# Performance work log

Hardware: AMD Instinct MI355X
Metric: run time of the kernel (lower is better)

## Reference

```python
import jax, jax.numpy as jnp
import numpy as np

CHOOSE_K = 256
NUM_CLASSES = 100
ALPHA = 0.1  # teacher-loss margin (Kaiser et al.)
EPS = 1e-12


def setup_inputs() -> dict:
    key = jax.random.key(0)
    k1, k2, k3, k4 = jax.random.split(key, 4)
    B, D, M, C = 512, 256, 131072, 100
    x = jax.random.normal(k1, (B, D), dtype=jnp.float32)
    y = jax.random.randint(k2, (B,), 0, C)
    mem_keys = jax.random.normal(k3, (M, D), dtype=jnp.float32)
    mem_vals = jax.random.randint(k4, (M,), 0, C)
    return {"x": x, "y": y, "mem_keys": mem_keys, "mem_vals": mem_vals}


def reference(x, y, mem_keys, mem_vals):
    # L2-normalize queries and memory keys (cosine similarity memory)
    qn = x / (jnp.linalg.norm(x, axis=-1, keepdims=True) + EPS)          # [B, D]
    kn = mem_keys / (jnp.linalg.norm(mem_keys, axis=-1, keepdims=True) + EPS)  # [M, D]

    sims = jnp.einsum('bd,md->bm', qn, kn)                                # [B, M]
    top_sims, top_idx = jax.lax.top_k(sims, CHOOSE_K)                     # [B, K]
    top_labels = mem_vals[top_idx]                                        # [B, K]

    # nearest-neighbor label
    closest_label = top_labels[:, 0]                                      # [B]

    # softmax over top-k similarities, scattered into class buckets
    w = jax.nn.softmax(top_sims, axis=-1)                                 # [B, K]
    onehot = jax.nn.one_hot(top_labels, NUM_CLASSES, dtype=w.dtype)       # [B, K, C]
    probs = jnp.einsum('bk,bkc->bc', w, onehot)                           # [B, C]

    # teacher loss: margin between nearest negative and nearest positive neighbor
    pos = top_labels == y[:, None]                                        # [B, K]
    sim_pos = jnp.max(jnp.where(pos, top_sims, -2.0), axis=1)             # [B]
    sim_neg = jnp.max(jnp.where(~pos, top_sims, -2.0), axis=1)            # [B]
    teacher_loss = jax.nn.relu(sim_neg - sim_pos + ALPHA)                 # [B]

    return closest_label, probs, teacher_loss
```

## Files before the change

### kernel.cpp

```cpp
#include <hip/hip_runtime.h>
#include <hip/hip_bf16.h>

#define NB 512
#define ND 256
#define NM 131072
#define NC 100
#define KTOP 256
#define ALPHA 0.1f
#define EPSN 1e-12
#define THRESH 0.155f
#define CUTBAND 0.012f
#define LCH 24
#define NCH 128
#define NSLOT (NCH*LCH)
#define IDXMASK 0x1FFFFu

typedef __attribute__((ext_vector_type(8))) short bf16x8;
typedef __attribute__((ext_vector_type(4))) float f32x4;

__global__ void zero_out_kernel(float* __restrict__ out, int n) {
    int t = blockIdx.x * blockDim.x + threadIdx.x;
    if (t < n) out[t] = 0.0f;
}

static __device__ __forceinline__ unsigned pk2(float a, float b) {
    __hip_bfloat16 ha = __float2bfloat16(a);
    __hip_bfloat16 hb = __float2bfloat16(b);
    unsigned short ua = __builtin_bit_cast(unsigned short, ha);
    unsigned short ub = __builtin_bit_cast(unsigned short, hb);
    return (unsigned)ua | ((unsigned)ub << 16);
}

static __device__ __forceinline__ void gload16(const void* g, const void* l) {
    __builtin_amdgcn_global_load_lds(
        (const __attribute__((address_space(1))) unsigned int*)g,
        (__attribute__((address_space(3))) unsigned int*)l, 16, 0, 0);
}

__global__ void norms_kernel(const float* __restrict__ x, const float* __restrict__ keys,
                             float* __restrict__ rnq32, float* __restrict__ rnk32,
                             double* __restrict__ rnq64, double* __restrict__ rnk64,
                             unsigned short* __restrict__ kb16) {
    int wave = (blockIdx.x * blockDim.x + threadIdx.x) >> 6;
    int lane = threadIdx.x & 63;
    if (wave >= NB + NM) return;
    const float* src = (wave < NB) ? (x + (size_t)wave * ND)
                                   : (keys + (size_t)(wave - NB) * ND);
    float4 v = ((const float4*)src)[lane];
    if (kb16 && wave >= NB) {
        size_t r = (size_t)(wave - NB);
        int kb = (lane << 3) ^ (((int)r & 7) << 4);
        *(uint2*)((char*)kb16 + (r << 9) + kb) =
            make_uint2(pk2(v.x, v.y), pk2(v.z, v.w));
    }
    double s = (double)v.x * v.x + (double)v.y * v.y
             + (double)v.z * v.z + (double)v.w * v.w;
    #pragma unroll
    for (int off = 32; off > 0; off >>= 1) s += __shfl_down(s, off);
    if (lane == 0) {
        double r = 1.0 / (sqrt(s) + EPSN);
        if (wave < NB) { rnq32[wave] = (float)r; rnq64[wave] = r; }
        else           { rnk32[wave - NB] = (float)r; rnk64[wave - NB] = r; }
    }
}

__global__ __launch_bounds__(512) void gemm_filter_pipe(
    const float* __restrict__ x, const unsigned short* __restrict__ kb16,
    const float* __restrict__ rnq, const float* __restrict__ rnk,
    float* __restrict__ cval, unsigned* __restrict__ cidx) {
    __shared__ unsigned short ks3[3][32 * 256];
    __shared__ unsigned lcnt[128];

    int tid  = threadIdx.x;
    int lane = tid & 63;
    int wv   = tid >> 6;
    int wr   = wv >> 1;
    int wc   = (wv & 1) * 16;
    int l15  = lane & 15;
    int lhi  = lane >> 4;
    int kxor = (l15 & 7) << 4;
    int chunk = blockIdx.x;
    int m0    = blockIdx.y * 128;

    if (tid < 128) lcnt[tid] = 0;

    bf16x8 af[2][8];
    #pragma unroll
    for (int mi = 0; mi < 2; ++mi) {
        const float* qp = x + (size_t)(m0 + wr * 32 + mi * 16 + l15) * ND;
        #pragma unroll
        for (int k8 = 0; k8 < 8; ++k8) {
            float4 qa = *(const float4*)(qp + k8 * 32 + lhi * 8);
            float4 qb = *(const float4*)(qp + k8 * 32 + lhi * 8 + 4);
            uint4 uu = make_uint4(pk2(qa.x, qa.y), pk2(qa.z, qa.w),
                                  pk2(qb.x, qb.y), pk2(qb.z, qb.w));
            af[mi][k8] = __builtin_bit_cast(bf16x8, uu);
        }
    }
    float rq[2][4];
    #pragma unroll
    for (int mi = 0; mi < 2; ++mi)
        #pragma unroll
        for (int j = 0; j < 4; ++j)
            rq[mi][j] = rnq[m0 + wr * 32 + mi * 16 + lhi * 4 + j];

    const char* kroot = (const char*)kb16 + ((size_t)chunk << 19);
    int sbase = wv << 11;

    #define STAGEP(T, B)                                                        \
    {                                                                           \
        const char* kb_ = kroot + ((size_t)(T) << 14);                          \
        gload16(kb_ + sbase + (lane << 4),        (const char*)&ks3[(B)][0] + sbase);        \
        gload16(kb_ + sbase + 1024 + (lane << 4), (const char*)&ks3[(B)][0] + sbase + 1024); \
    }

    #define COMPUTEP(T, BC)                                                     \
    {                                                                           \
        int n0 = chunk * 1024 + (T) * 32;                                       \
        const char* bb = (const char*)&ks3[(BC)][0];                            \
        f32x4 acc0 = {}, acc1 = {};                                             \
        _Pragma("unroll")                                                       \
        for (int k8 = 0; k8 < 8; ++k8) {                                        \
            int addr = ((wc + l15) << 9) + (((k8 << 6) + (lhi << 4)) ^ kxor);   \
            bf16x8 bg = *(const bf16x8*)(bb + addr);                            \
            acc0 = __builtin_amdgcn_mfma_f32_16x16x32_bf16(af[0][k8], bg, acc0, 0, 0, 0); \
            acc1 = __builtin_amdgcn_mfma_f32_16x16x32_bf16(af[1][k8], bg, acc1, 0, 0, 0); \
        }                                                                       \
        float rk = rnk[n0 + wc + l15];                                          \
        unsigned key = (unsigned)(n0 + wc + l15);                               \
        _Pragma("unroll")                                                       \
        for (int j = 0; j < 4; ++j) {                                           \
            float s0 = acc0[j] * rq[0][j] * rk;                                 \
            float s1 = acc1[j] * rq[1][j] * rk;                                 \
            int rl0 = wr * 32 + lhi * 4 + j;                                    \
            if (s0 > THRESH) {                                                  \
                unsigned p = atomicAdd(&lcnt[rl0], 1u);                         \
                if (p < LCH) {                                                  \
                    size_t slot = (size_t)(m0 + rl0) * NSLOT + (size_t)chunk * LCH + p; \
                    cval[slot] = s0; cidx[slot] = key;                          \
                }                                                               \
            }                                                                   \
            if (s1 > THRESH) {                                                  \
                unsigned p = atomicAdd(&lcnt[rl0 + 16], 1u);                    \
                if (p < LCH) {                                                  \
                    size_t slot = (size_t)(m0 + rl0 + 16) * NSLOT + (size_t)chunk * LCH + p; \
                    cval[slot] = s1; cidx[slot] = key;                          \
                }                                                               \
            }                                                                   \
        }                                                                       \
    }

    STAGEP(0, 0);
    STAGEP(1, 1);

    int bs = 2, bc = 0;
    for (int t = 0; t < 31; ++t) {
        asm volatile("s_waitcnt vmcnt(2)" ::: "memory");
        __builtin_amdgcn_sched_barrier(0);
        asm volatile("s_barrier" ::: "memory");
        __builtin_amdgcn_sched_barrier(0);
        COMPUTEP(t, bc);
        bc = (bc == 2) ? 0 : bc + 1;
        if (t < 30) {
            STAGEP(t + 2, bs);
            bs = (bs == 2) ? 0 : bs + 1;
        }
    }
    asm volatile("s_waitcnt vmcnt(0)" ::: "memory");
    __builtin_amdgcn_sched_barrier(0);
    asm volatile("s_barrier" ::: "memory");
    __builtin_amdgcn_sched_barrier(0);
    COMPUTEP(31, bc);
    __syncthreads();

    #undef STAGEP
    #undef COMPUTEP

    if (tid < 128) {
        unsigned c = lcnt[tid]; if (c > LCH) c = LCH;
        size_t base = (size_t)(m0 + tid) * NSLOT + (size_t)chunk * LCH;
        for (unsigned p = c; p < LCH; ++p) { cval[base + p] = -2.0f; cidx[base + p] = 0u; }
    }
}

#define LDKF 264

__global__ __launch_bounds__(512) void gemm_filter(
    const float* __restrict__ x, const float* __restrict__ keys,
    const float* __restrict__ rnq, const float* __restrict__ rnk,
    float* __restrict__ cval, unsigned* __restrict__ cidx) {
    __shared__ unsigned short ks[128][LDKF];
    __shared__ unsigned lcnt[128];

    int tid  = threadIdx.x;
    int lane = tid & 63;
    int wv   = tid >> 6;
    int wr4  = (wv >> 1) * 32;
    int wc2  = (wv &  1) * 64;
    int l15  = lane & 15;
    int lhi  = lane >> 4;
    int chunk = blockIdx.x;
    int m0    = blockIdx.y * 128;

    if (tid < 128) lcnt[tid] = 0;

    bf16x8 af[2][8];
    #pragma unroll
    for (int mi = 0; mi < 2; ++mi) {
        const float* qp = x + (size_t)(m0 + wr4 + mi * 16 + l15) * ND;
        #pragma unroll
        for (int k8 = 0; k8 < 8; ++k8) {
            float4 qa = *(const float4*)(qp + k8 * 32 + lhi * 8);
            float4 qb = *(const float4*)(qp + k8 * 32 + lhi * 8 + 4);
            uint4 uu = make_uint4(pk2(qa.x, qa.y), pk2(qa.z, qa.w),
                                  pk2(qb.x, qb.y), pk2(qb.z, qb.w));
            af[mi][k8] = __builtin_bit_cast(bf16x8, uu);
        }
    }
    float rq[2][4];
    #pragma unroll
    for (int mi = 0; mi < 2; ++mi)
        #pragma unroll
        for (int j = 0; j < 4; ++j)
            rq[mi][j] = rnq[m0 + wr4 + mi * 16 + lhi * 4 + j];

    for (int sub = 0; sub < 8; ++sub) {
        int n0 = chunk * 1024 + sub * 128;
        #pragma unroll 8
        for (int it = 0; it < 16; ++it) {
            int f = tid + it * 512;
            int r = f >> 6;
            int c4 = (f & 63) << 2;
            float4 kv = *(const float4*)(keys + (size_t)(n0 + r) * ND + c4);
            *(uint2*)&ks[r][c4] = make_uint2(pk2(kv.x, kv.y), pk2(kv.z, kv.w));
        }
        __syncthreads();

        f32x4 acc[2][4] = {};
        #pragma unroll
        for (int k8 = 0; k8 < 8; ++k8) {
            int ko = k8 * 32 + lhi * 8;
            bf16x8 bg[4];
            #pragma unroll
            for (int ni = 0; ni < 4; ++ni)
                bg[ni] = *(const bf16x8*)&ks[wc2 + ni * 16 + l15][ko];
            #pragma unroll
            for (int mi = 0; mi < 2; ++mi)
                #pragma unroll
                for (int ni = 0; ni < 4; ++ni)
                    acc[mi][ni] = __builtin_amdgcn_mfma_f32_16x16x32_bf16(
                        af[mi][k8], bg[ni], acc[mi][ni], 0, 0, 0);
        }

        float rk[4];
        #pragma unroll
        for (int ni = 0; ni < 4; ++ni) rk[ni] = rnk[n0 + wc2 + ni * 16 + l15];

        #pragma unroll
        for (int mi = 0; mi < 2; ++mi) {
            #pragma unroll
            for (int j = 0; j < 4; ++j) {
                int rl = wr4 + mi * 16 + lhi * 4 + j;
                #pragma unroll
                for (int ni = 0; ni < 4; ++ni) {
                    float sim = acc[mi][ni][j] * rq[mi][j] * rk[ni];
                    if (sim > THRESH) {
                        unsigned p = atomicAdd(&lcnt[rl], 1u);
                        if (p < LCH) {
                            size_t slot = (size_t)(m0 + rl) * NSLOT + (size_t)chunk * LCH + p;
                            cval[slot] = sim;
                            cidx[slot] = (unsigned)(n0 + wc2 + ni * 16 + l15);
                        }
                    }
                }
            }
        }
        __syncthreads();
    }

    if (tid < 128) {
        unsigned c = lcnt[tid]; if (c > LCH) c = LCH;
        size_t base = (size_t)(m0 + tid) * NSLOT + (size_t)chunk * LCH;
        for (unsigned p = c; p < LCH; ++p) { cval[base + p] = -2.0f; cidx[base + p] = 0u; }
    }
}

__global__ __launch_bounds__(512) void finalize(
    const float* __restrict__ cval, const unsigned* __restrict__ cidx,
    const float* __restrict__ x, const float* __restrict__ keys,
    const double* __restrict__ rnq64, const double* __restrict__ rnk64,
    const int* __restrict__ mem_vals, const int* __restrict__ yv,
    float* __restrict__ out) {
    int row = blockIdx.x;
    int tid = threadIdx.x;
    int lane = tid & 63;
    int wv8  = tid >> 6;

    __shared__ double xqd[ND];
    __shared__ double dval[NSLOT];
    __shared__ unsigned skid[NSLOT];
    __shared__ unsigned char flag[NSLOT];
    __shared__ unsigned hist[256];
    __shared__ unsigned eqlist[256];
    __shared__ float bins[128];
    __shared__ double wred_v[8];
    __shared__ unsigned wred_i[8];
    __shared__ double wred_se[8], wred_sp[8], wred_sn[8];
    __shared__ unsigned long long sh_prefix;
    __shared__ unsigned sh_k, eqcnt, ncand;
    __shared__ unsigned selA, kA;
    __shared__ float s_cut;
    __shared__ double s_vm;
    __shared__ unsigned s_im;
    __shared__ float s_se;
    __shared__ double s_sp, s_sn;

    if (tid == 0) {
        ncand = 0; eqcnt = 0; sh_k = KTOP; sh_prefix = 0x3F00000000000000ull;
        selA = 0xFFFFFFFFu; s_cut = 0.0f;
    }
    if (tid < 64) {
        float4 q = ((const float4*)(x + (size_t)row * ND))[tid];
        xqd[tid * 4 + 0] = (double)q.x; xqd[tid * 4 + 1] = (double)q.y;
        xqd[tid * 4 + 2] = (double)q.z; xqd[tid * 4 + 3] = (double)q.w;
    }
    __syncthreads();

    double rq = rnq64[row];

    if (tid < 256) hist[tid] = 0;
    __syncthreads();
    for (int i = tid; i < NSLOT; i += 512) {
        float v = cval[(size_t)row * NSLOT + i];
        if (v > 0.0f) atomicAdd(&hist[(__float_as_uint(v) >> 23) & 255u], 1u);
    }
    __syncthreads();
    for (int off = 1; off < 256; off <<= 1) {
        unsigned vv = 0;
        if (tid < 256) vv = hist[tid] + ((tid + off < 256) ? hist[tid + off] : 0u);
        __syncthreads();
        if (tid < 256) hist[tid] = vv;
        __syncthreads();
    }
    if (tid < 256) {
        unsigned rh = hist[tid];
        unsigned rn = (tid < 255) ? hist[tid + 1] : 0u;
        if (rh >= KTOP && rn < KTOP) { selA = (unsigned)tid; kA = KTOP - rn; }
    }
    __syncthreads();
    if (selA != 0xFFFFFFFFu) {
        unsigned sA = selA, kk = kA;
        if (tid < 256) hist[tid] = 0;
        __syncthreads();
        for (int i = tid; i < NSLOT; i += 512) {
            float v = cval[(size_t)row * NSLOT + i];
            if (v > 0.0f) {
                unsigned u = __float_as_uint(v);
                if (((u >> 23) & 255u) == sA) atomicAdd(&hist[(u >> 15) & 255u], 1u);
            }
        }
        __syncthreads();
        for (int off = 1; off < 256; off <<= 1) {
            unsigned vv = 0;
            if (tid < 256) vv = hist[tid] + ((tid + off < 256) ? hist[tid + off] : 0u);
            __syncthreads();
            if (tid < 256) hist[tid] = vv;
            __syncthreads();
        }
        if (tid < 256) {
            unsigned rh = hist[tid];
            unsigned rn = (tid < 255) ? hist[tid + 1] : 0u;
            if (rh >= kk && rn < kk)
                s_cut = __uint_as_float((sA << 23) | ((unsigned)tid << 15));
        }
        __syncthreads();
    }
    float cutf = (selA != 0xFFFFFFFFu) ? (s_cut - CUTBAND) : 0.0f;

    for (int i = tid; i < NSLOT; i += 512) {
        float v = cval[(size_t)row * NSLOT + i];
        if (v > cutf) {
            unsigned p = atomicAdd(&ncand, 1u);
            skid[p] = cidx[(size_t)row * NSLOT + i] & IDXMASK;
        }
    }
    __syncthreads();
    int nc = (int)ncand;

    for (int c0 = tid * 2; c0 < nc; c0 += 1024) {
        int c1 = c0 + 1;
        bool h1 = (c1 < nc);
        unsigned id0 = skid[c0];
        unsigned id1 = h1 ? skid[c1] : id0;
        const float* kp0 = keys + (size_t)id0 * ND;
        const float* kp1 = keys + (size_t)id1 * ND;
        double a0 = 0, a1 = 0, a2 = 0, a3 = 0;
        double b0 = 0, b1 = 0, b2 = 0, b3 = 0;
        #pragma unroll 4
        for (int d = 0; d < ND; d += 4) {
            float4 kv0 = *(const float4*)(kp0 + d);
            float4 kv1 = *(const float4*)(kp1 + d);
            double x0 = xqd[d + 0], x1 = xqd[d + 1], x2 = xqd[d + 2], x3 = xqd[d + 3];
            a0 = fma(x0, (double)kv0.x, a0);
            a1 = fma(x1, (double)kv0.y, a1);
            a2 = fma(x2, (double)kv0.z, a2);
            a3 = fma(x3, (double)kv0.w, a3);
            b0 = fma(x0, (double)kv1.x, b0);
            b1 = fma(x1, (double)kv1.y, b1);
            b2 = fma(x2, (double)kv1.z, b2);
            b3 = fma(x3, (double)kv1.w, b3);
        }
        dval[c0] = ((a0 + a1) + (a2 + a3)) * rq * rnk64[id0];
        if (h1) dval[c1] = ((b0 + b1) + (b2 + b3)) * rq * rnk64[id1];
    }
    __syncthreads();

    for (int pass = 1; pass < 8; ++pass) {
        int shift = 56 - pass * 8;
        unsigned long long mask_hi = ~0ull << (shift + 8);
        unsigned long long pfx = sh_prefix;
        unsigned kcur = sh_k;
        if (tid < 256) hist[tid] = 0;
        __syncthreads();
        for (int c = tid; c < nc; c += 512) {
            unsigned long long u = (unsigned long long)__double_as_longlong(dval[c]);
            if ((u & mask_hi) == pfx)
                atomicAdd(&hist[(unsigned)(u >> shift) & 255u], 1u);
        }
        __syncthreads();
        for (int off = 1; off < 256; off <<= 1) {
            unsigned v = 0;
            if (tid < 256) v = hist[tid] + ((tid + off < 256) ? hist[tid + off] : 0u);
            __syncthreads();
            if (tid < 256) hist[tid] = v;
            __syncthreads();
        }
        if (tid < 256) {
            unsigned rh = hist[tid];
            unsigned rn = (tid < 255) ? hist[tid + 1] : 0u;
            if (rh >= kcur && rn < kcur) {
                sh_prefix = pfx | ((unsigned long long)tid << shift);
                sh_k = kcur - rn;
            }
        }
        __syncthreads();
    }
    unsigned long long T = sh_prefix;
    unsigned need = sh_k;

    for (int c = tid; c < nc; c += 512) {
        unsigned long long u = (unsigned long long)__double_as_longlong(dval[c]);
        unsigned char f = 0;
        if (u > T) f = 1;
        else if (u == T) {
            unsigned p = atomicAdd(&eqcnt, 1u);
            if (p < 256u) eqlist[p] = (unsigned)c;
        }
        flag[c] = f;
    }
    __syncthreads();
    if (tid == 0) {
        unsigned ec = (eqcnt < 256u) ? eqcnt : 256u;
        if (ec <= need) {
            for (unsigned e = 0; e < ec; ++e) { unsigned ix = eqlist[e]; if (ix < NSLOT) flag[ix] = 1; }
        } else {
            for (unsigned t = 0; t < need; ++t) {
                unsigned best = 0xFFFFFFFFu, bp = 0;
                for (unsigned e = 0; e < ec; ++e) {
                    unsigned ci = eqlist[e];
                    if (ci < NSLOT && skid[ci] < best) { best = skid[ci]; bp = e; }
                }
                unsigned ix = eqlist[bp];
                if (ix < NSLOT) flag[ix] = 1;
                eqlist[bp] = 0xFFFFFFFFu;
            }
        }
    }
    if (tid < 128) bins[tid] = 0.0f;
    __syncthreads();

    double mv = -2.0; unsigned mi = IDXMASK;
    for (int c = tid; c < nc; c += 512) {
        double v = dval[c]; unsigned id = skid[c];
        if (v > mv || (v == mv && id < mi)) { mv = v; mi = id; }
    }
    #pragma unroll
    for (int off = 32; off > 0; off >>= 1) {
        double ov = __shfl_down(mv, off);
        unsigned oi = __shfl_down(mi, off);
        if (ov > mv || (ov == mv && oi < mi)) { mv = ov; mi = oi; }
    }
    if (lane == 0) { wred_v[wv8] = mv; wred_i[wv8] = mi; }
    __syncthreads();
    if (tid == 0) {
        double bv = wred_v[0]; unsigned bi = wred_i[0];
        for (int w = 1; w < 8; ++w) {
            double v2 = wred_v[w]; unsigned i2 = wred_i[w];
            if (v2 > bv || (v2 == bv && i2 < bi)) { bv = v2; bi = i2; }
        }
        s_vm = bv; s_im = bi & IDXMASK;
    }
    __syncthreads();
    double vmax = s_vm;
    unsigned imax = s_im;

    int yr = yv[row];
    float se = 0.0f;
    double sp = -2.0, sn = -2.0;
    for (int c = tid; c < nc; c += 512) {
        if (!flag[c]) continue;
        double v = dval[c];
        int lbl = mem_vals[skid[c]] & 127;
        float e = expf((float)(v - vmax));
        se += e;
        atomicAdd(&bins[lbl], e);
        if (lbl == yr) { if (v > sp) sp = v; }
        else           { if (v > sn) sn = v; }
    }
    double dse = (double)se;
    #pragma unroll
    for (int off = 32; off > 0; off >>= 1) {
        dse += __shfl_down(dse, off);
        double osp = __shfl_down(sp, off);
        double osn = __shfl_down(sn, off);
        sp = fmax(sp, osp);
        sn = fmax(sn, osn);
    }
    if (lane == 0) { wred_se[wv8] = dse; wred_sp[wv8] = sp; wred_sn[wv8] = sn; }
    __syncthreads();
    if (tid == 0) {
        double tse = wred_se[0], tsp = wred_sp[0], tsn = wred_sn[0];
        for (int w = 1; w < 8; ++w) {
            tse += wred_se[w];
            tsp = fmax(tsp, wred_sp[w]);
            tsn = fmax(tsn, wred_sn[w]);
        }
        s_se = fmaxf((float)tse, 1e-30f);
        s_sp = tsp; s_sn = tsn;
    }
    __syncthreads();

    if (tid < NC) {
        out[NB + (size_t)row * NC + tid] = bins[tid] / s_se;
    }
    if (tid == 0) {
        out[row] = (float)mem_vals[imax];
        double loss = s_sn - s_sp + (double)ALPHA;
        out[NB + (size_t)NB * NC + row] = (loss > 0.0) ? (float)loss : 0.0f;
    }
}

extern "C" void kernel_launch(void* const* d_in, const int* in_sizes, int n_in,
                              void* d_out, int out_size, void* d_ws, size_t ws_size,
                              hipStream_t stream) {
    const float* x    = (const float*)d_in[0];
    const int*   y    = (const int*)d_in[1];
    const float* keys = (const float*)d_in[2];
    const int*   mv   = (const int*)d_in[3];
    float* out = (float*)d_out;

    constexpr size_t WS_NEEDED = 14161920;
    constexpr size_t WS_BF16   = WS_NEEDED + (size_t)NM * ND * 2;
    if (ws_size < WS_NEEDED) {
        hipLaunchKernelGGL(zero_out_kernel, dim3((out_size + 255) / 256), dim3(256), 0, stream,
                           out, out_size);
        return;
    }

    char* ws = (char*)d_ws;
    float*    rnq32 = (float*)(ws + 0);
    float*    rnk32 = (float*)(ws + 2048);
    double*   rnq64 = (double*)(ws + 526336);
    double*   rnk64 = (double*)(ws + 530432);
    float*    cval  = (float*)(ws + 1579008);
    unsigned* cidx  = (unsigned*)(ws + 7870464);
    unsigned short* kb16 = (unsigned short*)(ws + WS_NEEDED);

    bool use_bf16 = (ws_size >= WS_BF16);
    hipLaunchKernelGGL(norms_kernel, dim3((NB + NM + 3) / 4), dim3(256), 0, stream,
                       x, keys, rnq32, rnk32, rnq64, rnk64,
                       use_bf16 ? kb16 : (unsigned short*)nullptr);
    if (use_bf16) {
        hipLaunchKernelGGL(gemm_filter_pipe, dim3(NCH, NB / 128), dim3(512), 0, stream,
                           x, kb16, rnq32, rnk32, cval, cidx);
    } else {
        hipLaunchKernelGGL(gemm_filter, dim3(NCH, NB / 128), dim3(512), 0, stream,
                           x, keys, rnq32, rnk32, cval, cidx);
    }
    hipLaunchKernelGGL(finalize, dim3(NB), dim3(512), 0, stream,
                       cval, cidx, x, keys, rnq64, rnk64, mv, y, out);
}
```

Baseline: 338.0 us.

## Replace 7-pass radix select with brute-force rank counting over candidates

Drops the multi-pass 8-bit radix select on the double-precision candidate sims, along with its serial tie-breaking on thread 0. Each candidate now computes its exact rank by comparing against every other candidate, with ties broken by index, and is flagged if the rank is below K. The aim is to remove the many barrier-heavy histogram and prefix-scan passes. The new step costs O(nc^2) shared-memory reads per row, which could be expensive if the candidate count is large. The fp64 dot-product loop is also reduced from two candidates per thread to one.

```diff
diff --git a/kernel.cpp b/kernel.cpp
--- a/kernel.cpp
+++ b/kernel.cpp
@@ -301,13 +301,11 @@
     __shared__ unsigned skid[NSLOT];
     __shared__ unsigned char flag[NSLOT];
     __shared__ unsigned hist[256];
-    __shared__ unsigned eqlist[256];
     __shared__ float bins[128];
     __shared__ double wred_v[8];
     __shared__ unsigned wred_i[8];
     __shared__ double wred_se[8], wred_sp[8], wred_sn[8];
-    __shared__ unsigned long long sh_prefix;
-    __shared__ unsigned sh_k, eqcnt, ncand;
+    __shared__ unsigned ncand;
     __shared__ unsigned selA, kA;
     __shared__ float s_cut;
     __shared__ double s_vm;
@@ -315,10 +313,7 @@
     __shared__ float s_se;
     __shared__ double s_sp, s_sn;
 
-    if (tid == 0) {
-        ncand = 0; eqcnt = 0; sh_k = KTOP; sh_prefix = 0x3F00000000000000ull;
-        selA = 0xFFFFFFFFu; s_cut = 0.0f;
-    }
+    if (tid == 0) { ncand = 0; selA = 0xFFFFFFFFu; s_cut = 0.0f; }
     if (tid < 64) {
         float4 q = ((const float4*)(x + (size_t)row * ND))[tid];
         xqd[tid * 4 + 0] = (double)q.x; xqd[tid * 4 + 1] = (double)q.y;
@@ -387,94 +382,31 @@
     __syncthreads();
     int nc = (int)ncand;
 
-    for (int c0 = tid * 2; c0 < nc; c0 += 1024) {
-        int c1 = c0 + 1;
-        bool h1 = (c1 < nc);
-        unsigned id0 = skid[c0];
-        unsigned id1 = h1 ? skid[c1] : id0;
+    for (int c = tid; c < nc; c += 512) {
+        unsigned id0 = skid[c];
         const float* kp0 = keys + (size_t)id0 * ND;
-        const float* kp1 = keys + (size_t)id1 * ND;
         double a0 = 0, a1 = 0, a2 = 0, a3 = 0;
-        double b0 = 0, b1 = 0, b2 = 0, b3 = 0;
         #pragma unroll 4
         for (int d = 0; d < ND; d += 4) {
             float4 kv0 = *(const float4*)(kp0 + d);
-            float4 kv1 = *(const float4*)(kp1 + d);
-            double x0 = xqd[d + 0], x1 = xqd[d + 1], x2 = xqd[d + 2], x3 = xqd[d + 3];
-            a0 = fma(x0, (double)kv0.x, a0);
-            a1 = fma(x1, (double)kv0.y, a1);
-            a2 = fma(x2, (double)kv0.z, a2);
-            a3 = fma(x3, (double)kv0.w, a3);
-            b0 = fma(x0, (double)kv1.x, b0);
-            b1 = fma(x1, (double)kv1.y, b1);
-            b2 = fma(x2, (double)kv1.z, b2);
-            b3 = fma(x3, (double)kv1.w, b3);
-        }
-        dval[c0] = ((a0 + a1) + (a2 + a3)) * rq * rnk64[id0];
-        if (h1) dval[c1] = ((b0 + b1) + (b2 + b3)) * rq * rnk64[id1];
-    }
-    __syncthreads();
-
-    for (int pass = 1; pass < 8; ++pass) {
-        int shift = 56 - pass * 8;
-        unsigned long long mask_hi = ~0ull << (shift + 8);
-        unsigned long long pfx = sh_prefix;
-        unsigned kcur = sh_k;
-        if (tid < 256) hist[tid] = 0;
-        __syncthreads();
-        for (int c = tid; c < nc; c += 512) {
-            unsigned long long u = (unsigned long long)__double_as_longlong(dval[c]);
-            if ((u & mask_hi) == pfx)
-                atomicAdd(&hist[(unsigned)(u >> shift) & 255u], 1u);
-        }
-        __syncthreads();
-        for (int off = 1; off < 256; off <<= 1) {
-            unsigned v = 0;
-            if (tid < 256) v = hist[tid] + ((tid + off < 256) ? hist[tid + off] : 0u);
-            __syncthreads();
-            if (tid < 256) hist[tid] = v;
-            __syncthreads();
-        }
-        if (tid < 256) {
-            unsigned rh = hist[tid];
-            unsigned rn = (tid < 255) ? hist[tid + 1] : 0u;
-            if (rh >= kcur && rn < kcur) {
-                sh_prefix = pfx | ((unsigned long long)tid << shift);
-                sh_k = kcur - rn;
-            }
-        }
-        __syncthreads();
-    }
-    unsigned long long T = sh_prefix;
-    unsigned need = sh_k;
+            a0 = fma(xqd[d + 0], (double)kv0.x, a0);
+            a1 = fma(xqd[d + 1], (double)kv0.y, a1);
+            a2 = fma(xqd[d + 2], (double)kv0.z, a2);
+            a3 = fma(xqd[d + 3], (double)kv0.w, a3);
+        }
+        dval[c] = ((a0 + a1) + (a2 + a3)) * rq * rnk64[id0];
+    }
+    __syncthreads();
 
     for (int c = tid; c < nc; c += 512) {
-        unsigned long long u = (unsigned long long)__double_as_longlong(dval[c]);
-        unsigned char f = 0;
-        if (u > T) f = 1;
-        else if (u == T) {
-            unsigned p = atomicAdd(&eqcnt, 1u);
-            if (p < 256u) eqlist[p] = (unsigned)c;
-        }
-        flag[c] = f;
-    }
-    __syncthreads();
-    if (tid == 0) {
-        unsigned ec = (eqcnt < 256u) ? eqcnt : 256u;
-        if (ec <= need) {
-            for (unsigned e = 0; e < ec; ++e) { unsigned ix = eqlist[e]; if (ix < NSLOT) flag[ix] = 1; }
-        } else {
-            for (unsigned t = 0; t < need; ++t) {
-                unsigned best = 0xFFFFFFFFu, bp = 0;
-                for (unsigned e = 0; e < ec; ++e) {
-                    unsigned ci = eqlist[e];
-                    if (ci < NSLOT && skid[ci] < best) { best = skid[ci]; bp = e; }
-                }
-                unsigned ix = eqlist[bp];
-                if (ix < NSLOT) flag[ix] = 1;
-                eqlist[bp] = 0xFFFFFFFFu;
-            }
-        }
+        unsigned long long uc = (unsigned long long)__double_as_longlong(dval[c]);
+        unsigned sc = skid[c];
+        unsigned rank = 0;
+        for (int j = 0; j < nc; ++j) {
+            unsigned long long uj = (unsigned long long)__double_as_longlong(dval[j]);
+            if (uj > uc || (uj == uc && skid[j] < sc)) ++rank;
+        }
+        flag[c] = (rank < KTOP) ? 1 : 0;
     }
     if (tid < 128) bins[tid] = 0.0f;
     __syncthreads();
```

Result: slower. 408.7 us (+20.9%).
